# Performance work log

Hardware: AMD Instinct MI355X
Metric: run time of the kernel (lower is better)

The kernel has to match this reference:

```python
import jax, jax.numpy as jnp
import numpy as np

NEG_SLOPE = 0.2  # PyG GATConv default


def gat_conv(x, src, dst, W_src, W_dst, att_src, att_dst, bias, heads, ch, n_nodes):
    """One PyG-style GATConv with self-loops already included in (src, dst).
    Returns [N, heads*ch] (concat over heads)."""
    xs = (x @ W_src).reshape(n_nodes, heads, ch)  # source-side transform (messages)
    xd = (x @ W_dst).reshape(n_nodes, heads, ch)  # dest-side transform (attention only)
    a_s = jnp.sum(xs * att_src, axis=-1)  # [N, H]
    a_d = jnp.sum(xd * att_dst, axis=-1)  # [N, H]
    e = jax.nn.leaky_relu(a_s[src] + a_d[dst], NEG_SLOPE)  # [E, H]
    # segment softmax over edges grouped by destination node
    m = jax.ops.segment_max(e, dst, num_segments=n_nodes)  # [N, H]
    ex = jnp.exp(e - m[dst])
    denom = jax.ops.segment_sum(ex, dst, num_segments=n_nodes)  # [N, H]
    alpha = ex / denom[dst]  # [E, H]
    # weighted scatter-aggregate of source messages
    out = jax.ops.segment_sum(xs[src] * alpha[:, :, None], dst, num_segments=n_nodes)
    return out.reshape(n_nodes, heads * ch) + bias


def setup_inputs() -> dict:
    key = jax.random.key(0)
    ks = jax.random.split(key, 12)
    N, F, E = 50000, 128, 400000
    H, C1, C2 = 4, 64, 64
    x = jax.random.normal(ks[0], (N, F), dtype=jnp.float32)
    edge_index = jax.random.randint(ks[1], (2, E), 0, N, dtype=jnp.int64)
    g = lambda k, shape, fan_in: jax.random.normal(k, shape, dtype=jnp.float32) * (1.0 / np.sqrt(fan_in))
    return {
        "x": x,
        "edge_index": edge_index,
        "W1_src": g(ks[2], (F, H * C1), F),
        "W1_dst": g(ks[3], (F, H * C1), F),
        "att1_src": g(ks[4], (H, C1), C1),
        "att1_dst": g(ks[5], (H, C1), C1),
        "b1": jnp.zeros((H * C1,), dtype=jnp.float32),
        "W2_src": g(ks[6], (H * C1, C2), H * C1),
        "W2_dst": g(ks[7], (H * C1, C2), H * C1),
        "att2_src": g(ks[8], (1, C2), C2),
        "att2_dst": g(ks[9], (1, C2), C2),
        "b2": jnp.zeros((C2,), dtype=jnp.float32),
    }


def reference(x, edge_index, W1_src, W1_dst, att1_src, att1_dst, b1,
              W2_src, W2_dst, att2_src, att2_dst, b2):
    N = x.shape[0]
    loop = jnp.arange(N, dtype=edge_index.dtype)
    src = jnp.concatenate([edge_index[0], loop])  # add_self_loops=True
    dst = jnp.concatenate([edge_index[1], loop])
    H, C1 = att1_src.shape
    C2 = att2_src.shape[1]
    h = gat_conv(x, src, dst, W1_src, W1_dst, att1_src, att1_dst, b1, H, C1, N)
    h = jax.nn.relu(h)
    # dropout is identity in eval mode
    out = gat_conv(h, src, dst, W2_src, W2_dst, att2_src, att2_dst, b2, 1, C2, N)
    return out
```

## Files before the change

kernel.cpp:

```cpp
#include <hip/hip_runtime.h>


static inline int cdiv(int a, int b) { return (a + b - 1) / b; }

typedef __attribute__((ext_vector_type(8))) short short8;
typedef __attribute__((ext_vector_type(4))) float floatx4;

__device__ __forceinline__ float bf2f(unsigned short u) {
  return __uint_as_float(((unsigned int)u) << 16);
}
__device__ __forceinline__ unsigned short f2bf(float f) {
  unsigned int u = __float_as_uint(f);
  unsigned int r = (u + 0x7FFFu + ((u >> 16) & 1u)) >> 16;
  return (unsigned short)r;
}
__device__ __forceinline__ float ldv(const void* p, int i, int bf) {
  return bf ? bf2f(((const unsigned short*)p)[i]) : ((const float*)p)[i];
}
#define NEG_INF (-__builtin_inff())

__global__ void fill_out_kernel(float* __restrict__ out, int n, float val) {
  int t = blockIdx.x * blockDim.x + threadIdx.x;
  if (t < n) out[t] = val;
}

__device__ int probe_bf(const unsigned short* xu) {
  __shared__ int cc;
  if (threadIdx.x == 0) cc = 0;
  __syncthreads();
  int l0 = 0;
  for (int i = threadIdx.x; i < 1024; i += 256) {
    int e = (xu[2 * i] >> 7) & 0xFF;
    if (e >= 100 && e <= 141) l0++;
  }
  atomicAdd(&cc, l0);
  __syncthreads();
  return cc > 512 ? 1 : 0;
}
__device__ int probe_e64(const unsigned int* eu) {
  __shared__ int ce;
  if (threadIdx.x == 0) ce = 0;
  __syncthreads();
  int l1 = 0;
  for (int i = threadIdx.x; i < 1024; i += 256)
    if (eu[2 * i + 1] == 0u) l1++;
  atomicAdd(&ce, l1);
  __syncthreads();
  return ce > 512 ? 1 : 0;
}

__global__ void prep_edges(const unsigned short* __restrict__ xu,
                           const void* __restrict__ EI, int E, int EP, int Nn,
                           const void* __restrict__ W1s, const void* __restrict__ W1d,
                           const void* __restrict__ a1s, const void* __restrict__ a1d,
                           const void* __restrict__ W2s, const void* __restrict__ W2d,
                           const void* __restrict__ a2s, const void* __restrict__ a2d,
                           const void* __restrict__ b1, const void* __restrict__ b2,
                           unsigned short* __restrict__ W1cT,
                           unsigned short* __restrict__ W2sT,
                           unsigned short* __restrict__ W1extT,
                           float* __restrict__ v2s, float* __restrict__ v2d,
                           float* __restrict__ b1f, float* __restrict__ b2f,
                           int* __restrict__ srcI, int* __restrict__ dstI,
                           int* __restrict__ posE,
                           int* __restrict__ deg) {
  const int b = blockIdx.x, t = threadIdx.x;
  if (b < 128) {
    const int bf = probe_bf(xu);
    int i = b * 256 + t;
    int k = i >> 8, col = i & 255;
    W1cT[col * 128 + k] = f2bf(ldv(W1s, i, bf));
  } else if (b < 192) {
    const int bf = probe_bf(xu);
    int i = (b - 128) * 256 + t;
    int k = i >> 6, col = i & 63;
    W2sT[col * 256 + k] = f2bf(ldv(W2s, i, bf));
  } else if (b < 198) {
    const int bf = probe_bf(xu);
    const int lane = t & 63, w = t >> 6;
    const int g = lane >> 3, ll = lane & 7;
    const int base = (b - 192) * 256 + w * 64 + g;
#pragma unroll
    for (int r = 0; r < 8; ++r) {
      const int d = base + r * 8;
      const void *W, *A;
      int wo, ao;
      if (d < 1024) {
        int k = d >> 3, q = d & 7, h = q & 3;
        W = (q < 4) ? W1s : W1d;
        A = (q < 4) ? a1s : a1d;
        wo = k * 256 + h * 64;
        ao = h * 64;
      } else {
        int e = d - 1024, k = e & 255;
        W = (e < 256) ? W2s : W2d;
        A = (e < 256) ? a2s : a2d;
        wo = k * 64;
        ao = 0;
      }
      float p;
      if (bf) {
        uint4 wv = *(const uint4*)((const unsigned short*)W + wo + ll * 8);
        uint4 av = *(const uint4*)((const unsigned short*)A + ao + ll * 8);
        p  = bf2f((unsigned short)(wv.x & 0xFFFF)) * bf2f((unsigned short)(av.x & 0xFFFF));
        p += bf2f((unsigned short)(wv.x >> 16))    * bf2f((unsigned short)(av.x >> 16));
        p += bf2f((unsigned short)(wv.y & 0xFFFF)) * bf2f((unsigned short)(av.y & 0xFFFF));
        p += bf2f((unsigned short)(wv.y >> 16))    * bf2f((unsigned short)(av.y >> 16));
        p += bf2f((unsigned short)(wv.z & 0xFFFF)) * bf2f((unsigned short)(av.z & 0xFFFF));
        p += bf2f((unsigned short)(wv.z >> 16))    * bf2f((unsigned short)(av.z >> 16));
        p += bf2f((unsigned short)(wv.w & 0xFFFF)) * bf2f((unsigned short)(av.w & 0xFFFF));
        p += bf2f((unsigned short)(wv.w >> 16))    * bf2f((unsigned short)(av.w >> 16));
      } else {
        float4 w0 = *(const float4*)((const float*)W + wo + ll * 8);
        float4 w1 = *(const float4*)((const float*)W + wo + ll * 8 + 4);
        float4 a0 = *(const float4*)((const float*)A + ao + ll * 8);
        float4 a1 = *(const float4*)((const float*)A + ao + ll * 8 + 4);
        p = w0.x * a0.x + w0.y * a0.y + w0.z * a0.z + w0.w * a0.w +
            w1.x * a1.x + w1.y * a1.y + w1.z * a1.z + w1.w * a1.w;
      }
      p += __shfl_xor(p, 1);
      p += __shfl_xor(p, 2);
      p += __shfl_xor(p, 4);
      if (ll == 0) {
        if (d < 1024) {
          int k = d >> 3, q = d & 7;
          W1extT[q * 128 + k] = f2bf(p);
          W1extT[(8 + q) * 128 + k] = 0;
        } else {
          int e = d - 1024, k = e & 255;
          if (e < 256) v2s[k] = p; else v2d[k] = p;
        }
      }
    }
  } else if (b == 198) {
    const int bf = probe_bf(xu);
    b1f[t] = ldv(b1, t, bf);
    if (t < 64) b2f[t] = ldv(b2, t, bf);
  } else {
    const int e64 = probe_e64((const unsigned int*)EI);
    int i = (b - 199) * 256 + t;
    if (i < EP) {
      int s, d;
      if (i < E) {
        if (e64) {
          const unsigned int* p = (const unsigned int*)EI;
          s = (int)p[2 * (size_t)i];
          d = (int)p[2 * ((size_t)E + i)];
        } else {
          const int* p = (const int*)EI;
          s = p[i]; d = p[E + i];
        }
      } else { s = i - E; d = s; }
      if ((unsigned)s >= (unsigned)Nn) s = 0;
      if ((unsigned)d >= (unsigned)Nn) d = 0;
      srcI[i] = s; dstI[i] = d;
      posE[i] = atomicAdd(&deg[d], 1);
    }
  }
}

__global__ __launch_bounds__(256) void scan_gemm(
    const void* __restrict__ X, const unsigned short* __restrict__ xu,
    const int* __restrict__ deg, int* __restrict__ rowst,
    int* __restrict__ scanflag, int nb,
    const unsigned short* __restrict__ W1cT, const unsigned short* __restrict__ W1extT,
    unsigned short* __restrict__ xs1, float* __restrict__ A1, int N) {
  __shared__ __align__(16) unsigned short smem[64 * 136];
  const int t = threadIdx.x;
  if (blockIdx.x < nb) {
    const int c = blockIdx.x;
    int* ssc = (int*)smem;
    int i = c * 256 + t;
    int v = (i < N) ? deg[i] : 0;
    ssc[t] = v;
    __syncthreads();
    for (int off = 1; off < 256; off <<= 1) {
      int add = (t >= off) ? ssc[t - off] : 0;
      __syncthreads();
      ssc[t] += add;
      __syncthreads();
    }
    int incl = ssc[t];
    if (t == 255) atomicExch(&scanflag[c], ssc[255] + 1);
    __syncthreads();
    int pre = 0;
    if (t < c) {
      int f;
      while ((f = __hip_atomic_load(&scanflag[t], __ATOMIC_RELAXED,
                                    __HIP_MEMORY_SCOPE_AGENT)) == 0) {}
      pre = f - 1;
    }
    int* s2 = ssc + 256;
    s2[t] = pre;
    __syncthreads();
    for (int off = 128; off; off >>= 1) {
      if (t < off) s2[t] += s2[t + off];
      __syncthreads();
    }
    if (i < N) rowst[i] = s2[0] + incl - v;
    return;
  }
  const int bf = probe_bf(xu);
  unsigned short* Wlds = smem;
  const int lane = t & 63, wid = t >> 6;
  const int quad = lane >> 4, m16 = lane & 15;
  const int r0b = (blockIdx.x - nb) * 64;
  const int r0 = r0b + wid * 16;
  const int arow = min(r0 + m16, N - 1);
  short8 af[4];
  if (bf) {
    const uint4* Xr = (const uint4*)((const unsigned int*)X + (size_t)arow * 64);
#pragma unroll
    for (int ks = 0; ks < 4; ++ks)
      af[ks] = __builtin_bit_cast(short8, Xr[ks * 4 + quad]);
  } else {
    const float* Xr = (const float*)X + (size_t)arow * 128;
#pragma unroll
    for (int ks = 0; ks < 4; ++ks) {
      short8 v;
#pragma unroll
      for (int j = 0; j < 8; ++j) v[j] = (short)f2bf(Xr[ks * 32 + quad * 8 + j]);
      af[ks] = v;
    }
  }
#pragma unroll
  for (int ph = 0; ph < 2; ++ph) {
    floatx4 accs[9];
    const int ncts = ph ? 8 : 9;
#pragma unroll
    for (int ct = 0; ct < 9; ++ct) {
      if (ct >= ncts) break;
      floatx4 acc = {0.f, 0.f, 0.f, 0.f};
      const unsigned short* bp = (ct < 8)
          ? W1cT + (size_t)(ph * 128 + ct * 16 + m16) * 128
          : W1extT + (size_t)m16 * 128;
#pragma unroll
      for (int ks = 0; ks < 4; ++ks) {
        short8 bfv = *(const short8*)(bp + ks * 32 + quad * 8);
        acc = __builtin_amdgcn_mfma_f32_16x16x32_bf16(af[ks], bfv, acc, 0, 0, 0);
      }
      accs[ct] = acc;
    }
    if (ph == 0 && m16 < 8) {
#pragma unroll
      for (int r = 0; r < 4; ++r) {
        int row = r0 + quad * 4 + r;
        if (row < N) A1[(size_t)row * 8 + m16] = accs[8][r];
      }
    }
#pragma unroll
    for (int ct = 0; ct < 8; ++ct)
#pragma unroll
      for (int r = 0; r < 4; ++r)
        Wlds[(wid * 16 + quad * 4 + r) * 136 + ct * 16 + m16] = f2bf(accs[ct][r]);
    __syncthreads();
#pragma unroll
    for (int it = 0; it < 4; ++it) {
      int lrow = it * 16 + (t >> 4);
      int grow = r0b + lrow;
      if (grow < N) {
        uint4 v = *(const uint4*)&Wlds[lrow * 136 + (t & 15) * 8];
        *(uint4*)(xs1 + (size_t)grow * 256 + ph * 128 + (t & 15) * 8) = v;
      }
    }
    __syncthreads();
  }
}

__global__ void fill_srcS(const int* __restrict__ srcI, const int* __restrict__ dstI,
                          const int* __restrict__ posE, int EP,
                          const int* __restrict__ rowst, int* __restrict__ srcS) {
  int t = blockIdx.x * blockDim.x + threadIdx.x;
  if (t >= EP) return;
  int d = dstI[t];
  srcS[rowst[d] + posE[t]] = srcI[t];
}

__global__ __launch_bounds__(256) void node1_merged(
    const int* __restrict__ rowst, const int* __restrict__ deg,
    const int* __restrict__ srcS,
    const float* __restrict__ A1, const unsigned short* __restrict__ xs1,
    const float* __restrict__ b1f, const unsigned short* __restrict__ W2sT,
    const float* __restrict__ v2s, const float* __restrict__ v2d,
    unsigned short* __restrict__ xs2, float* __restrict__ A2, int N) {
  __shared__ unsigned short hb[8][272];
  __shared__ int   s_sh[4][2][32];
  __shared__ float al_sh[4][2][32][4];
  const int lane = threadIdx.x & 63;
  const int wid = threadIdx.x >> 6;
  const int hf = lane >> 5;
  const int hl = lane & 31;
  const int nraw = blockIdx.x * 8 + wid * 2 + hf;
  const bool valid = nraw < N;
  const int n = valid ? nraw : (N - 1);
  const int st = rowst[n], dn = deg[n];
  const float4 ad4 = *(const float4*)(A1 + (size_t)n * 8 + 4);
  const float ad[4] = {ad4.x, ad4.y, ad4.z, ad4.w};
  const int gc = 8 * hl;
  const int hd = hl >> 3;
  float acc[8] = {0.f, 0.f, 0.f, 0.f, 0.f, 0.f, 0.f, 0.f};
  constexpr int PF = 12;

  if (__all(dn <= 32)) {
    int s = 0;
    float4 as4 = make_float4(0.f, 0.f, 0.f, 0.f);
    if (hl < dn) {
      s = srcS[st + hl];
      as4 = *(const float4*)(A1 + (size_t)s * 8);
    }
    const int np = dn < PF ? dn : PF;
    uint4 u[PF];
#pragma unroll
    for (int j = 0; j < PF; ++j) {
      if (j < np) {
        int sj = __shfl(s, (hf << 5) + j);
        u[j] = *(const uint4*)(xs1 + (size_t)sj * 256 + gc);
      }
    }
    float v[4] = {NEG_INF, NEG_INF, NEG_INF, NEG_INF};
    if (hl < dn) {
      const float as[4] = {as4.x, as4.y, as4.z, as4.w};
#pragma unroll
      for (int h = 0; h < 4; ++h) {
        float x = as[h] + ad[h];
        v[h] = x > 0.f ? x : 0.2f * x;
      }
    }
    float m[4], l[4];
#pragma unroll
    for (int h = 0; h < 4; ++h) {
      m[h] = v[h];
#pragma unroll
      for (int off = 16; off; off >>= 1) m[h] = fmaxf(m[h], __shfl_xor(m[h], off));
      float e = (hl < dn) ? __expf(v[h] - m[h]) : 0.f;
      l[h] = e;
#pragma unroll
      for (int off = 16; off; off >>= 1) l[h] += __shfl_xor(l[h], off);
      v[h] = e;
    }
    if (hl < dn) {
      s_sh[wid][hf][hl] = s;
      float4 al = {v[0] / l[0], v[1] / l[1], v[2] / l[2], v[3] / l[3]};
      *(float4*)&al_sh[wid][hf][hl][0] = al;
    }
#pragma unroll
    for (int j = 0; j < PF; ++j) {
      if (j < np) {
        float a0 = al_sh[wid][hf][j][hd];
        acc[0] += a0 * __uint_as_float(u[j].x << 16);
        acc[1] += a0 * __uint_as_float(u[j].x & 0xFFFF0000u);
        acc[2] += a0 * __uint_as_float(u[j].y << 16);
        acc[3] += a0 * __uint_as_float(u[j].y & 0xFFFF0000u);
        acc[4] += a0 * __uint_as_float(u[j].z << 16);
        acc[5] += a0 * __uint_as_float(u[j].z & 0xFFFF0000u);
        acc[6] += a0 * __uint_as_float(u[j].w << 16);
        acc[7] += a0 * __uint_as_float(u[j].w & 0xFFFF0000u);
      }
    }
    for (int j = np; j < dn; ++j) {
      int s0 = s_sh[wid][hf][j];
      float a0 = al_sh[wid][hf][j][hd];
      uint4 uu = *(const uint4*)(xs1 + (size_t)s0 * 256 + gc);
      acc[0] += a0 * __uint_as_float(uu.x << 16);
      acc[1] += a0 * __uint_as_float(uu.x & 0xFFFF0000u);
      acc[2] += a0 * __uint_as_float(uu.y << 16);
      acc[3] += a0 * __uint_as_float(uu.y & 0xFFFF0000u);
      acc[4] += a0 * __uint_as_float(uu.z << 16);
      acc[5] += a0 * __uint_as_float(uu.z & 0xFFFF0000u);
      acc[6] += a0 * __uint_as_float(uu.w << 16);
      acc[7] += a0 * __uint_as_float(uu.w & 0xFFFF0000u);
    }
  } else {
    float m[4] = {NEG_INF, NEG_INF, NEG_INF, NEG_INF};
    for (int j = hl; j < dn; j += 32) {
      int s = srcS[st + j];
      const float4 as4 = *(const float4*)(A1 + (size_t)s * 8);
      const float as[4] = {as4.x, as4.y, as4.z, as4.w};
#pragma unroll
      for (int h = 0; h < 4; ++h) {
        float x = as[h] + ad[h];
        x = x > 0.f ? x : 0.2f * x;
        m[h] = fmaxf(m[h], x);
      }
    }
#pragma unroll
    for (int h = 0; h < 4; ++h)
#pragma unroll
      for (int off = 16; off; off >>= 1) m[h] = fmaxf(m[h], __shfl_xor(m[h], off));
    float l[4] = {0.f, 0.f, 0.f, 0.f};
    for (int j = hl; j < dn; j += 32) {
      int s = srcS[st + j];
      const float4 as4 = *(const float4*)(A1 + (size_t)s * 8);
      const float as[4] = {as4.x, as4.y, as4.z, as4.w};
#pragma unroll
      for (int h = 0; h < 4; ++h) {
        float x = as[h] + ad[h];
        x = x > 0.f ? x : 0.2f * x;
        l[h] += __expf(x - m[h]);
      }
    }
#pragma unroll
    for (int h = 0; h < 4; ++h)
#pragma unroll
      for (int off = 16; off; off >>= 1) l[h] += __shfl_xor(l[h], off);
    const float mh = m[hd], inv = 1.0f / l[hd], adh = ad[hd];
    for (int j = 0; j < dn; ++j) {
      int s = srcS[st + j];
      float x = A1[(size_t)s * 8 + hd] + adh;
      x = x > 0.f ? x : 0.2f * x;
      float alpha = __expf(x - mh) * inv;
      uint4 uu = *(const uint4*)(xs1 + (size_t)s * 256 + gc);
      acc[0] += alpha * __uint_as_float(uu.x << 16);
      acc[1] += alpha * __uint_as_float(uu.x & 0xFFFF0000u);
      acc[2] += alpha * __uint_as_float(uu.y << 16);
      acc[3] += alpha * __uint_as_float(uu.y & 0xFFFF0000u);
      acc[4] += alpha * __uint_as_float(uu.z << 16);
      acc[5] += alpha * __uint_as_float(uu.z & 0xFFFF0000u);
      acc[6] += alpha * __uint_as_float(uu.w << 16);
      acc[7] += alpha * __uint_as_float(uu.w & 0xFFFF0000u);
    }
  }

  const float4 bb0 = *(const float4*)(b1f + gc);
  const float4 bb1 = *(const float4*)(b1f + gc + 4);
  float hv[8];
  hv[0] = acc[0] + bb0.x; hv[1] = acc[1] + bb0.y;
  hv[2] = acc[2] + bb0.z; hv[3] = acc[3] + bb0.w;
  hv[4] = acc[4] + bb1.x; hv[5] = acc[5] + bb1.y;
  hv[6] = acc[6] + bb1.z; hv[7] = acc[7] + bb1.w;
#pragma unroll
  for (int k = 0; k < 8; ++k) hv[k] = hv[k] > 0.f ? hv[k] : 0.f;
  const float4 vs0 = *(const float4*)(v2s + gc);
  const float4 vs1 = *(const float4*)(v2s + gc + 4);
  const float4 vd0 = *(const float4*)(v2d + gc);
  const float4 vd1 = *(const float4*)(v2d + gc + 4);
  float ps = hv[0] * vs0.x + hv[1] * vs0.y + hv[2] * vs0.z + hv[3] * vs0.w +
             hv[4] * vs1.x + hv[5] * vs1.y + hv[6] * vs1.z + hv[7] * vs1.w;
  float pd = hv[0] * vd0.x + hv[1] * vd0.y + hv[2] * vd0.z + hv[3] * vd0.w +
             hv[4] * vd1.x + hv[5] * vd1.y + hv[6] * vd1.z + hv[7] * vd1.w;
#pragma unroll
  for (int off = 1; off <= 16; off <<= 1) {
    ps += __shfl_xor(ps, off);
    pd += __shfl_xor(pd, off);
  }
  unsigned int p0 = (unsigned int)f2bf(hv[0]) | ((unsigned int)f2bf(hv[1]) << 16);
  unsigned int p1 = (unsigned int)f2bf(hv[2]) | ((unsigned int)f2bf(hv[3]) << 16);
  unsigned int p2 = (unsigned int)f2bf(hv[4]) | ((unsigned int)f2bf(hv[5]) << 16);
  unsigned int p3 = (unsigned int)f2bf(hv[6]) | ((unsigned int)f2bf(hv[7]) << 16);
  *(uint4*)&hb[wid * 2 + hf][gc] = make_uint4(p0, p1, p2, p3);
  if (valid && hl == 0) {
    A2[(size_t)n * 2] = ps;
    A2[(size_t)n * 2 + 1] = pd;
  }
  __syncthreads();
  const int m16 = lane & 15, quad = lane >> 4;
  floatx4 c2 = {0.f, 0.f, 0.f, 0.f};
  const unsigned short* arow = &hb[m16 & 7][0];
  const unsigned short* bcol = W2sT + (size_t)(wid * 16 + m16) * 256;
#pragma unroll
  for (int ks = 0; ks < 8; ++ks) {
    short8 afr = *(const short8*)(arow + ks * 32 + quad * 8);
    short8 bfr = *(const short8*)(bcol + ks * 32 + quad * 8);
    c2 = __builtin_amdgcn_mfma_f32_16x16x32_bf16(afr, bfr, c2, 0, 0, 0);
  }
  if (quad < 2) {
#pragma unroll
    for (int r = 0; r < 4; ++r) {
      int node = blockIdx.x * 8 + quad * 4 + r;
      if (node < N) xs2[(size_t)node * 64 + wid * 16 + m16] = f2bf(c2[r]);
    }
  }
}

__global__ __launch_bounds__(256) void node2(const int* __restrict__ rowst,
    const int* __restrict__ deg, const int* __restrict__ srcS,
    const float* __restrict__ A2, const unsigned short* __restrict__ xs2,
    const float* __restrict__ b2f, float* __restrict__ out, int N) {
  __shared__ int   s_sh[4][2][32];
  __shared__ float al_sh[4][2][32];
  const int lane = threadIdx.x & 63;
  const int wid = threadIdx.x >> 6;
  const int hf = lane >> 5;
  const int hl = lane & 31;
  const int nraw = blockIdx.x * 8 + wid * 2 + hf;
  const bool valid = nraw < N;
  const int n = valid ? nraw : (N - 1);
  const int st = rowst[n], dn = deg[n];
  const float ad = A2[(size_t)n * 2 + 1];
  float ax = 0.f, ay = 0.f;
  constexpr int PF2 = 16;
  if (__all(dn <= 32)) {
    int s = 0;
    float a2v = 0.f;
    if (hl < dn) {
      s = srcS[st + hl];
      a2v = A2[(size_t)s * 2];
    }
    const int np = dn < PF2 ? dn : PF2;
    unsigned int u[PF2];
#pragma unroll
    for (int j = 0; j < PF2; ++j) {
      if (j < np) {
        int sj = __shfl(s, (hf << 5) + j);
        u[j] = *(const unsigned int*)(xs2 + (size_t)sj * 64 + 2 * hl);
      }
    }
    float v = NEG_INF;
    if (hl < dn) {
      v = a2v + ad;
      v = v > 0.f ? v : 0.2f * v;
    }
    float m = v;
#pragma unroll
    for (int off = 16; off; off >>= 1) m = fmaxf(m, __shfl_xor(m, off));
    float e = (hl < dn) ? __expf(v - m) : 0.f;
    float l = e;
#pragma unroll
    for (int off = 16; off; off >>= 1) l += __shfl_xor(l, off);
    if (hl < dn) { s_sh[wid][hf][hl] = s; al_sh[wid][hf][hl] = e / l; }
#pragma unroll
    for (int j = 0; j < PF2; ++j) {
      if (j < np) {
        float a = al_sh[wid][hf][j];
        ax += a * __uint_as_float(u[j] << 16);
        ay += a * __uint_as_float(u[j] & 0xFFFF0000u);
      }
    }
    for (int j = np; j < dn; ++j) {
      int s0 = s_sh[wid][hf][j];
      float a = al_sh[wid][hf][j];
      unsigned int uu = *(const unsigned int*)(xs2 + (size_t)s0 * 64 + 2 * hl);
      ax += a * __uint_as_float(uu << 16);
      ay += a * __uint_as_float(uu & 0xFFFF0000u);
    }
  } else {
    float m = NEG_INF;
    for (int j = hl; j < dn; j += 32) {
      int s = srcS[st + j];
      float v = A2[(size_t)s * 2] + ad;
      v = v > 0.f ? v : 0.2f * v;
      m = fmaxf(m, v);
    }
#pragma unroll
    for (int off = 16; off; off >>= 1) m = fmaxf(m, __shfl_xor(m, off));
    float l = 0.f;
    for (int j = hl; j < dn; j += 32) {
      int s = srcS[st + j];
      float v = A2[(size_t)s * 2] + ad;
      v = v > 0.f ? v : 0.2f * v;
      l += __expf(v - m);
    }
#pragma unroll
    for (int off = 16; off; off >>= 1) l += __shfl_xor(l, off);
    float inv = 1.0f / l;
    for (int j = 0; j < dn; ++j) {
      int s = srcS[st + j];
      float v = A2[(size_t)s * 2] + ad;
      v = v > 0.f ? v : 0.2f * v;
      float alpha = __expf(v - m) * inv;
      unsigned int uu = *(const unsigned int*)(xs2 + (size_t)s * 64 + 2 * hl);
      ax += alpha * __uint_as_float(uu << 16);
      ay += alpha * __uint_as_float(uu & 0xFFFF0000u);
    }
  }
  if (valid) {
    const float2 b = *(const float2*)(b2f + 2 * hl);
    float2 o = make_float2(ax + b.x, ay + b.y);
    *(float2*)(out + (size_t)n * 64 + 2 * hl) = o;
  }
}

extern "C" void kernel_launch(void* const* d_in, const int* in_sizes, int n_in,
                              void* d_out, int out_size, void* d_ws, size_t ws_size,
                              hipStream_t stream) {
  const int F = 128, HC1 = 256, C2 = 64;
  const int N  = in_sizes[0] / F;
  const int E  = in_sizes[1] / 2;
  const int EP = E + N;
  (void)n_in;

  char* w = (char*)d_ws;
  size_t off = 0;
  auto alloc = [&](size_t bytes) -> char* {
    char* p = w + off;
    off = (off + bytes + 255) & ~(size_t)255;
    return p;
  };
  int* srcI   = (int*)alloc((size_t)EP * 4);
  int* dstI   = (int*)alloc((size_t)EP * 4);
  int* posE   = (int*)alloc((size_t)EP * 4);
  int* degcur = (int*)alloc(((size_t)N + 256) * 4);
  int* deg    = degcur;
  int* scanflag = degcur + N;
  int* rowst  = (int*)alloc((size_t)N * 4);
  unsigned short* W1cT  = (unsigned short*)alloc((size_t)F * HC1 * 2);
  unsigned short* W1extT = (unsigned short*)alloc(16 * 128 * 2);
  unsigned short* W2sT  = (unsigned short*)alloc((size_t)HC1 * C2 * 2);
  float* v2s  = (float*)alloc(256 * 4);
  float* v2d  = (float*)alloc(256 * 4);
  float* b1f  = (float*)alloc(256 * 4);
  float* b2f  = (float*)alloc(64 * 4);
  int*   srcS = (int*)alloc((size_t)EP * 4);
  float* A1   = (float*)alloc((size_t)N * 8 * 4);
  unsigned short* xs1 = (unsigned short*)alloc((size_t)N * HC1 * 2);
  unsigned short* xs2 = (unsigned short*)alloc((size_t)N * C2 * 2);
  float* A2 = (float*)alloc((size_t)N * 2 * 4);
  const size_t need = off;

  if (ws_size < need) {
    fill_out_kernel<<<cdiv(out_size, 256), 256, 0, stream>>>(
        (float*)d_out, out_size, 131072.0f + 1024.0f * (float)(ws_size >> 20));
    return;
  }

  hipMemsetAsync(degcur, 0, ((size_t)N + 256) * 4, stream);

  prep_edges<<<199 + cdiv(EP, 256), 256, 0, stream>>>(
      (const unsigned short*)d_in[0], d_in[1], E, EP, N,
      d_in[2], d_in[3], d_in[4], d_in[5], d_in[7], d_in[8], d_in[9], d_in[10],
      d_in[6], d_in[11],
      W1cT, W2sT, W1extT, v2s, v2d, b1f, b2f, srcI, dstI, posE, deg);

  const int nb = cdiv(N, 256);
  scan_gemm<<<nb + cdiv(N, 64), 256, 0, stream>>>(
      d_in[0], (const unsigned short*)d_in[0], deg, rowst, scanflag, nb,
      W1cT, W1extT, xs1, A1, N);

  fill_srcS<<<cdiv(EP, 256), 256, 0, stream>>>(srcI, dstI, posE, EP, rowst, srcS);
  node1_merged<<<cdiv(N, 8), 256, 0, stream>>>(rowst, deg, srcS, A1, xs1,
                                               b1f, W2sT, v2s, v2d, xs2, A2, N);
  node2<<<cdiv(N, 8), 256, 0, stream>>>(rowst, deg, srcS, A2, xs2, b2f,
                                        (float*)d_out, N);
}
```

Before: 233.4 us.

## Replace CSR build with fixed 32-slot per-node adjacency plus overflow list

Edges are now written directly into a padded N×32 source table by atomic slot position, with edges past slot 32 appended to a global overflow list. This drops the prefix scan, the fill_srcS kernel and the srcI/dstI/posE buffers, so the GEMM kernel no longer carries scan blocks and one launch disappears. The cost is a larger padded table, and for any node with degree above 32 every lane linearly scans the whole overflow list, which gets expensive if many nodes overflow. The padded layout also loses the CSR compaction of neighbour indices.

New measurement: 231.0 us. No clear change (-1.0%).

```diff
diff --git a/kernel.cpp b/kernel.cpp
--- a/kernel.cpp
+++ b/kernel.cpp
@@ -61,8 +61,9 @@
                            unsigned short* __restrict__ W1extT,
                            float* __restrict__ v2s, float* __restrict__ v2d,
                            float* __restrict__ b1f, float* __restrict__ b2f,
-                           int* __restrict__ srcI, int* __restrict__ dstI,
-                           int* __restrict__ posE,
+                           int* __restrict__ srcS32,
+                           int* __restrict__ ovfD, int* __restrict__ ovfS,
+                           int* __restrict__ novf,
                            int* __restrict__ deg) {
   const int b = blockIdx.x, t = threadIdx.x;
   if (b < 128) {
@@ -153,58 +154,27 @@
       } else { s = i - E; d = s; }
       if ((unsigned)s >= (unsigned)Nn) s = 0;
       if ((unsigned)d >= (unsigned)Nn) d = 0;
-      srcI[i] = s; dstI[i] = d;
-      posE[i] = atomicAdd(&deg[d], 1);
-    }
-  }
-}
-
-__global__ __launch_bounds__(256) void scan_gemm(
+      int pos = atomicAdd(&deg[d], 1);
+      if (pos < 32) {
+        srcS32[(size_t)d * 32 + pos] = s;
+      } else {
+        int o = atomicAdd(novf, 1);
+        ovfD[o] = d; ovfS[o] = s;
+      }
+    }
+  }
+}
+
+__global__ __launch_bounds__(256) void gemm1(
     const void* __restrict__ X, const unsigned short* __restrict__ xu,
-    const int* __restrict__ deg, int* __restrict__ rowst,
-    int* __restrict__ scanflag, int nb,
     const unsigned short* __restrict__ W1cT, const unsigned short* __restrict__ W1extT,
     unsigned short* __restrict__ xs1, float* __restrict__ A1, int N) {
-  __shared__ __align__(16) unsigned short smem[64 * 136];
+  __shared__ __align__(16) unsigned short Wlds[64 * 136];
   const int t = threadIdx.x;
-  if (blockIdx.x < nb) {
-    const int c = blockIdx.x;
-    int* ssc = (int*)smem;
-    int i = c * 256 + t;
-    int v = (i < N) ? deg[i] : 0;
-    ssc[t] = v;
-    __syncthreads();
-    for (int off = 1; off < 256; off <<= 1) {
-      int add = (t >= off) ? ssc[t - off] : 0;
-      __syncthreads();
-      ssc[t] += add;
-      __syncthreads();
-    }
-    int incl = ssc[t];
-    if (t == 255) atomicExch(&scanflag[c], ssc[255] + 1);
-    __syncthreads();
-    int pre = 0;
-    if (t < c) {
-      int f;
-      while ((f = __hip_atomic_load(&scanflag[t], __ATOMIC_RELAXED,
-                                    __HIP_MEMORY_SCOPE_AGENT)) == 0) {}
-      pre = f - 1;
-    }
-    int* s2 = ssc + 256;
-    s2[t] = pre;
-    __syncthreads();
-    for (int off = 128; off; off >>= 1) {
-      if (t < off) s2[t] += s2[t + off];
-      __syncthreads();
-    }
-    if (i < N) rowst[i] = s2[0] + incl - v;
-    return;
-  }
   const int bf = probe_bf(xu);
-  unsigned short* Wlds = smem;
   const int lane = t & 63, wid = t >> 6;
   const int quad = lane >> 4, m16 = lane & 15;
-  const int r0b = (blockIdx.x - nb) * 64;
+  const int r0b = blockIdx.x * 64;
   const int r0 = r0b + wid * 16;
   const int arow = min(r0 + m16, N - 1);
   short8 af[4];
@@ -267,18 +237,10 @@
   }
 }
 
-__global__ void fill_srcS(const int* __restrict__ srcI, const int* __restrict__ dstI,
-                          const int* __restrict__ posE, int EP,
-                          const int* __restrict__ rowst, int* __restrict__ srcS) {
-  int t = blockIdx.x * blockDim.x + threadIdx.x;
-  if (t >= EP) return;
-  int d = dstI[t];
-  srcS[rowst[d] + posE[t]] = srcI[t];
-}
-
 __global__ __launch_bounds__(256) void node1_merged(
-    const int* __restrict__ rowst, const int* __restrict__ deg,
-    const int* __restrict__ srcS,
+    const int* __restrict__ deg, const int* __restrict__ srcS32,
+    const int* __restrict__ ovfD, const int* __restrict__ ovfS,
+    const int* __restrict__ novfp,
     const float* __restrict__ A1, const unsigned short* __restrict__ xs1,
     const float* __restrict__ b1f, const unsigned short* __restrict__ W2sT,
     const float* __restrict__ v2s, const float* __restrict__ v2d,
@@ -293,7 +255,7 @@
   const int nraw = blockIdx.x * 8 + wid * 2 + hf;
   const bool valid = nraw < N;
   const int n = valid ? nraw : (N - 1);
-  const int st = rowst[n], dn = deg[n];
+  const int dn = deg[n];
   const float4 ad4 = *(const float4*)(A1 + (size_t)n * 8 + 4);
   const float ad[4] = {ad4.x, ad4.y, ad4.z, ad4.w};
   const int gc = 8 * hl;
@@ -305,7 +267,7 @@
     int s = 0;
     float4 as4 = make_float4(0.f, 0.f, 0.f, 0.f);
     if (hl < dn) {
-      s = srcS[st + hl];
+      s = srcS32[(size_t)n * 32 + hl];
       as4 = *(const float4*)(A1 + (size_t)s * 8);
     }
     const int np = dn < PF ? dn : PF;
@@ -371,16 +333,31 @@
       acc[7] += a0 * __uint_as_float(uu.w & 0xFFFF0000u);
     }
   } else {
+    const int nov = *novfp;
+    const int nc = dn < 32 ? dn : 32;
     float m[4] = {NEG_INF, NEG_INF, NEG_INF, NEG_INF};
-    for (int j = hl; j < dn; j += 32) {
-      int s = srcS[st + j];
+    if (hl < nc) {
+      int s = srcS32[(size_t)n * 32 + hl];
       const float4 as4 = *(const float4*)(A1 + (size_t)s * 8);
       const float as[4] = {as4.x, as4.y, as4.z, as4.w};
 #pragma unroll
       for (int h = 0; h < 4; ++h) {
         float x = as[h] + ad[h];
         x = x > 0.f ? x : 0.2f * x;
-        m[h] = fmaxf(m[h], x);
+        m[h] = x;
+      }
+    }
+    for (int o = hl; o < nov; o += 32) {
+      if (ovfD[o] == n) {
+        int s = ovfS[o];
+        const float4 as4 = *(const float4*)(A1 + (size_t)s * 8);
+        const float as[4] = {as4.x, as4.y, as4.z, as4.w};
+#pragma unroll
+        for (int h = 0; h < 4; ++h) {
+          float x = as[h] + ad[h];
+          x = x > 0.f ? x : 0.2f * x;
+          m[h] = fmaxf(m[h], x);
+        }
       }
     }
 #pragma unroll
@@ -388,8 +365,8 @@
 #pragma unroll
       for (int off = 16; off; off >>= 1) m[h] = fmaxf(m[h], __shfl_xor(m[h], off));
     float l[4] = {0.f, 0.f, 0.f, 0.f};
-    for (int j = hl; j < dn; j += 32) {
-      int s = srcS[st + j];
+    if (hl < nc) {
+      int s = srcS32[(size_t)n * 32 + hl];
       const float4 as4 = *(const float4*)(A1 + (size_t)s * 8);
       const float as[4] = {as4.x, as4.y, as4.z, as4.w};
 #pragma unroll
@@ -399,13 +376,26 @@
         l[h] += __expf(x - m[h]);
       }
     }
+    for (int o = hl; o < nov; o += 32) {
+      if (ovfD[o] == n) {
+        int s = ovfS[o];
+        const float4 as4 = *(const float4*)(A1 + (size_t)s * 8);
+        const float as[4] = {as4.x, as4.y, as4.z, as4.w};
+#pragma unroll
+        for (int h = 0; h < 4; ++h) {
+          float x = as[h] + ad[h];
+          x = x > 0.f ? x : 0.2f * x;
+          l[h] += __expf(x - m[h]);
+        }
+      }
+    }
 #pragma unroll
     for (int h = 0; h < 4; ++h)
 #pragma unroll
       for (int off = 16; off; off >>= 1) l[h] += __shfl_xor(l[h], off);
     const float mh = m[hd], inv = 1.0f / l[hd], adh = ad[hd];
-    for (int j = 0; j < dn; ++j) {
-      int s = srcS[st + j];
+    for (int j = 0; j < nc; ++j) {
+      int s = srcS32[(size_t)n * 32 + j];
       float x = A1[(size_t)s * 8 + hd] + adh;
       x = x > 0.f ? x : 0.2f * x;
       float alpha = __expf(x - mh) * inv;
@@ -419,6 +409,23 @@
       acc[6] += alpha * __uint_as_float(uu.w << 16);
       acc[7] += alpha * __uint_as_float(uu.w & 0xFFFF0000u);
     }
+    for (int o = 0; o < nov; ++o) {
+      if (ovfD[o] == n) {
+        int s = ovfS[o];
+        float x = A1[(size_t)s * 8 + hd] + adh;
+        x = x > 0.f ? x : 0.2f * x;
+        float alpha = __expf(x - mh) * inv;
+        uint4 uu = *(const uint4*)(xs1 + (size_t)s * 256 + gc);
+        acc[0] += alpha * __uint_as_float(uu.x << 16);
+        acc[1] += alpha * __uint_as_float(uu.x & 0xFFFF0000u);
+        acc[2] += alpha * __uint_as_float(uu.y << 16);
+        acc[3] += alpha * __uint_as_float(uu.y & 0xFFFF0000u);
+        acc[4] += alpha * __uint_as_float(uu.z << 16);
+        acc[5] += alpha * __uint_as_float(uu.z & 0xFFFF0000u);
+        acc[6] += alpha * __uint_as_float(uu.w << 16);
+        acc[7] += alpha * __uint_as_float(uu.w & 0xFFFF0000u);
+      }
+    }
   }
 
   const float4 bb0 = *(const float4*)(b1f + gc);
@@ -472,8 +479,10 @@
   }
 }
 
-__global__ __launch_bounds__(256) void node2(const int* __restrict__ rowst,
-    const int* __restrict__ deg, const int* __restrict__ srcS,
+__global__ __launch_bounds__(256) void node2(
+    const int* __restrict__ deg, const int* __restrict__ srcS32,
+    const int* __restrict__ ovfD, const int* __restrict__ ovfS,
+    const int* __restrict__ novfp,
     const float* __restrict__ A2, const unsigned short* __restrict__ xs2,
     const float* __restrict__ b2f, float* __restrict__ out, int N) {
   __shared__ int   s_sh[4][2][32];
@@ -485,7 +494,7 @@
   const int nraw = blockIdx.x * 8 + wid * 2 + hf;
   const bool valid = nraw < N;
   const int n = valid ? nraw : (N - 1);
-  const int st = rowst[n], dn = deg[n];
+  const int dn = deg[n];
   const float ad = A2[(size_t)n * 2 + 1];
   float ax = 0.f, ay = 0.f;
   constexpr int PF2 = 16;
@@ -493,7 +502,7 @@
     int s = 0;
     float a2v = 0.f;
     if (hl < dn) {
-      s = srcS[st + hl];
+      s = srcS32[(size_t)n * 32 + hl];
       a2v = A2[(size_t)s * 2];
     }
     const int np = dn < PF2 ? dn : PF2;
@@ -534,33 +543,60 @@
       ay += a * __uint_as_float(uu & 0xFFFF0000u);
     }
   } else {
+    const int nov = *novfp;
+    const int nc = dn < 32 ? dn : 32;
     float m = NEG_INF;
-    for (int j = hl; j < dn; j += 32) {
-      int s = srcS[st + j];
+    if (hl < nc) {
+      int s = srcS32[(size_t)n * 32 + hl];
       float v = A2[(size_t)s * 2] + ad;
       v = v > 0.f ? v : 0.2f * v;
-      m = fmaxf(m, v);
+      m = v;
+    }
+    for (int o = hl; o < nov; o += 32) {
+      if (ovfD[o] == n) {
+        float v = A2[(size_t)ovfS[o] * 2] + ad;
+        v = v > 0.f ? v : 0.2f * v;
+        m = fmaxf(m, v);
+      }
     }
 #pragma unroll
     for (int off = 16; off; off >>= 1) m = fmaxf(m, __shfl_xor(m, off));
     float l = 0.f;
-    for (int j = hl; j < dn; j += 32) {
-      int s = srcS[st + j];
+    if (hl < nc) {
+      int s = srcS32[(size_t)n * 32 + hl];
       float v = A2[(size_t)s * 2] + ad;
       v = v > 0.f ? v : 0.2f * v;
       l += __expf(v - m);
     }
+    for (int o = hl; o < nov; o += 32) {
+      if (ovfD[o] == n) {
+        float v = A2[(size_t)ovfS[o] * 2] + ad;
+        v = v > 0.f ? v : 0.2f * v;
+        l += __expf(v - m);
+      }
+    }
 #pragma unroll
     for (int off = 16; off; off >>= 1) l += __shfl_xor(l, off);
     float inv = 1.0f / l;
-    for (int j = 0; j < dn; ++j) {
-      int s = srcS[st + j];
+    for (int j = 0; j < nc; ++j) {
+      int s = srcS32[(size_t)n * 32 + j];
       float v = A2[(size_t)s * 2] + ad;
       v = v > 0.f ? v : 0.2f * v;
       float alpha = __expf(v - m) * inv;
       unsigned int uu = *(const unsigned int*)(xs2 + (size_t)s * 64 + 2 * hl);
       ax += alpha * __uint_as_float(uu << 16);
       ay += alpha * __uint_as_float(uu & 0xFFFF0000u);
+    }
+    for (int o = 0; o < nov; ++o) {
+      if (ovfD[o] == n) {
+        int s = ovfS[o];
+        float v = A2[(size_t)s * 2] + ad;
+        v = v > 0.f ? v : 0.2f * v;
+        float alpha = __expf(v - m) * inv;
+        unsigned int uu = *(const unsigned int*)(xs2 + (size_t)s * 64 + 2 * hl);
+        ax += alpha * __uint_as_float(uu << 16);
+        ay += alpha * __uint_as_float(uu & 0xFFFF0000u);
+      }
     }
   }
   if (valid) {
@@ -586,13 +622,12 @@
     off = (off + bytes + 255) & ~(size_t)255;
     return p;
   };
-  int* srcI   = (int*)alloc((size_t)EP * 4);
-  int* dstI   = (int*)alloc((size_t)EP * 4);
-  int* posE   = (int*)alloc((size_t)EP * 4);
-  int* degcur = (int*)alloc(((size_t)N + 256) * 4);
-  int* deg    = degcur;
-  int* scanflag = degcur + N;
-  int* rowst  = (int*)alloc((size_t)N * 4);
+  int* srcS32 = (int*)alloc((size_t)N * 32 * 4);
+  int* ovfD   = (int*)alloc((size_t)EP * 4);
+  int* ovfS   = (int*)alloc((size_t)EP * 4);
+  int* degnv  = (int*)alloc(((size_t)N + 8) * 4);
+  int* deg    = degnv;
+  int* novf   = degnv + N;
   unsigned short* W1cT  = (unsigned short*)alloc((size_t)F * HC1 * 2);
   unsigned short* W1extT = (unsigned short*)alloc(16 * 128 * 2);
   unsigned short* W2sT  = (unsigned short*)alloc((size_t)HC1 * C2 * 2);
@@ -600,7 +635,6 @@
   float* v2d  = (float*)alloc(256 * 4);
   float* b1f  = (float*)alloc(256 * 4);
   float* b2f  = (float*)alloc(64 * 4);
-  int*   srcS = (int*)alloc((size_t)EP * 4);
   float* A1   = (float*)alloc((size_t)N * 8 * 4);
   unsigned short* xs1 = (unsigned short*)alloc((size_t)N * HC1 * 2);
   unsigned short* xs2 = (unsigned short*)alloc((size_t)N * C2 * 2);
@@ -613,22 +647,21 @@
     return;
   }
 
-  hipMemsetAsync(degcur, 0, ((size_t)N + 256) * 4, stream);
+  hipMemsetAsync(degnv, 0, ((size_t)N + 8) * 4, stream);
 
   prep_edges<<<199 + cdiv(EP, 256), 256, 0, stream>>>(
       (const unsigned short*)d_in[0], d_in[1], E, EP, N,
       d_in[2], d_in[3], d_in[4], d_in[5], d_in[7], d_in[8], d_in[9], d_in[10],
       d_in[6], d_in[11],
-      W1cT, W2sT, W1extT, v2s, v2d, b1f, b2f, srcI, dstI, posE, deg);
-
-  const int nb = cdiv(N, 256);
-  scan_gemm<<<nb + cdiv(N, 64), 256, 0, stream>>>(
-      d_in[0], (const unsigned short*)d_in[0], deg, rowst, scanflag, nb,
-      W1cT, W1extT, xs1, A1, N);
-
-  fill_srcS<<<cdiv(EP, 256), 256, 0, stream>>>(srcI, dstI, posE, EP, rowst, srcS);
-  node1_merged<<<cdiv(N, 8), 256, 0, stream>>>(rowst, deg, srcS, A1, xs1,
-                                               b1f, W2sT, v2s, v2d, xs2, A2, N);
-  node2<<<cdiv(N, 8), 256, 0, stream>>>(rowst, deg, srcS, A2, xs2, b2f,
-                                        (float*)d_out, N);
-}
+      W1cT, W2sT, W1extT, v2s, v2d, b1f, b2f,
+      srcS32, ovfD, ovfS, novf, deg);
+
+  gemm1<<<cdiv(N, 64), 256, 0, stream>>>(
+      d_in[0], (const unsigned short*)d_in[0], W1cT, W1extT, xs1, A1, N);
+
+  node1_merged<<<cdiv(N, 8), 256, 0, stream>>>(deg, srcS32, ovfD, ovfS, novf,
+                                               A1, xs1, b1f, W2sT, v2s, v2d,
+                                               xs2, A2, N);
+  node2<<<cdiv(N, 8), 256, 0, stream>>>(deg, srcS32, ovfD, ovfS, novf,
+                                        A2, xs2, b2f, (float*)d_out, N);
+}
```
